# Optimization experiments

Hardware: AMD Instinct MI355X
Metric: run time of the kernel (lower is better)

Reference implementation:

```python
import jax, jax.numpy as jnp
import numpy as np


def _forward(agent_qs, ally_states, enemy_states, W_al, b_al, W_en, b_en, Wq, bq, Wk, bk,
             w1_W1, w1_b1, w1_W2, w1_b2, wf_W1, wf_b1, wf_W2, wf_b2, hb_W, hb_b,
             v_W1, v_b1, v_W2, v_b2):
    A, B, S, _ = ally_states.shape
    E = A + enemy_states.shape[0]
    D = W_al.shape[1]
    Da = Wq.shape[1]
    # entity encoders: [A,B,S,D], [En,B,S,D]
    ally_embed = ally_states @ W_al + b_al
    enemy_embed = enemy_states @ W_en + b_en
    entity = jnp.concatenate([ally_embed, enemy_embed], axis=0)      # [E,B,S,D]
    ent_bs = jnp.transpose(entity, (1, 2, 0, 3))                     # [B,S,E,D]
    q = ent_bs @ Wq + bq                                             # [B,S,E,Da]
    k = ent_bs @ Wk + bk                                             # [B,S,E,Da]
    scale = jnp.asarray(Da, q.dtype) ** 0.5
    energy = jnp.einsum('bsid,bsjd->bsij', q / scale, k)             # [B,S,E,E]
    # torch softmax(dim=1) on [BS,E,E] == softmax over the query axis i
    attn = jax.nn.softmax(energy, axis=2)
    # bmm(value[BS,D,E], attn).mean(-1) == value @ mean_j attn[:, :, e, j]
    attn_mean = jnp.mean(attn, axis=3)                               # [B,S,E]
    attn_out = jnp.einsum('bsed,bse->bsd', ent_bs, attn_mean)        # [B,S,D]
    ally_bs = jnp.transpose(ally_embed, (1, 2, 0, 3))                # [B,S,A,D]
    emi = jnp.concatenate(
        [jnp.broadcast_to(attn_out[:, :, None, :], (B, S, A, D)), ally_bs], axis=-1)  # [B,S,A,2D]
    # hypernets (2-layer)
    w1 = jnp.abs(jax.nn.relu(emi @ w1_W1 + w1_b1) @ w1_W2 + w1_b2)   # [B,S,A,M]
    b1 = attn_out @ hb_W + hb_b                                      # [B,S,M]
    hidden = jax.nn.elu(jnp.einsum('bsa,bsam->bsm', agent_qs, w1) + b1)
    wf = jnp.abs(jax.nn.relu(attn_out @ wf_W1 + wf_b1) @ wf_W2 + wf_b2)  # [B,S,M]
    v = jax.nn.relu(attn_out @ v_W1 + v_b1) @ v_W2 + v_b2            # [B,S,1]
    q_tot = jnp.einsum('bsm,bsm->bs', hidden, wf)[..., None] + v     # [B,S,1]
    return q_tot


def setup_inputs() -> dict:
    key = jax.random.key(0)
    B, S, A, En = 128, 128, 8, 8
    NFal, NFen, D, Da, M, H = 32, 16, 64, 128, 32, 64
    ks = jax.random.split(key, 32)
    p = lambda i, shape: jax.random.normal(ks[i], shape, dtype=jnp.float32) * 0.05
    return dict(
        agent_qs=jax.random.normal(ks[0], (B, S, A), dtype=jnp.float32),
        ally_states=jax.random.normal(ks[1], (A, B, S, NFal), dtype=jnp.float32),
        enemy_states=jax.random.normal(ks[2], (En, B, S, NFen), dtype=jnp.float32),
        W_al=p(3, (NFal, D)), b_al=p(4, (D,)), W_en=p(5, (NFen, D)), b_en=p(6, (D,)),
        Wq=p(7, (D, Da)), bq=p(8, (Da,)), Wk=p(9, (D, Da)), bk=p(10, (Da,)),
        w1_W1=p(11, (2 * D, H)), w1_b1=p(12, (H,)), w1_W2=p(13, (H, M)), w1_b2=p(14, (M,)),
        wf_W1=p(15, (D, H)), wf_b1=p(16, (H,)), wf_W2=p(17, (H, M)), wf_b2=p(18, (M,)),
        hb_W=p(19, (D, M)), hb_b=p(20, (M,)),
        v_W1=p(21, (D, M)), v_b1=p(22, (M,)), v_W2=p(23, (M, 1)), v_b2=p(24, (1,)),
    )


def reference(agent_qs, ally_states, enemy_states, W_al, b_al, W_en, b_en, Wq, bq, Wk, bk,
              w1_W1, w1_b1, w1_W2, w1_b2, wf_W1, wf_b1, wf_W2, wf_b2, hb_W, hb_b,
              v_W1, v_b1, v_W2, v_b2):
    return _forward(agent_qs, ally_states, enemy_states, W_al, b_al, W_en, b_en, Wq, bq, Wk, bk,
                    w1_W1, w1_b1, w1_W2, w1_b2, wf_W1, wf_b1, wf_W2, wf_b2, hb_W, hb_b,
                    v_W1, v_b1, v_W2, v_b2)
```

## Files before the change

### kernel.cpp

```cpp
#include <hip/hip_runtime.h>
#include <hip/hip_bf16.h>


#define B_   128
#define S_   128
#define BS_  (B_ * S_)
#define WPB  2
#define INV_S 0.08838834764831845f

typedef short bs8 __attribute__((ext_vector_type(8)));
typedef float f4  __attribute__((ext_vector_type(4)));

#define MFMA(a, b, c) __builtin_amdgcn_mfma_f32_16x16x32_bf16((a), (b), (c), 0, 0, 0)
#define LOADB(t) (*(const bs8*)&fb[(size_t)(t) * 512 + lane * 8])

__device__ __forceinline__ short f2bf(float f) {
    union { float f; unsigned u; } v; v.f = f;
    unsigned r = v.u + 0x7fffu + ((v.u >> 16) & 1u);
    return (short)(r >> 16);
}

__global__ __launch_bounds__(64)
void qmix_pre1(const float* __restrict__ Wq, const float* __restrict__ Wk,
               const float* __restrict__ bk,
               float* __restrict__ Ms, float* __restrict__ vq)
{
    const int blk = blockIdx.x, t = threadIdx.x;
    float p;
    if (blk < 4096) {
        const int k = blk >> 6, n = blk & 63;
        p = Wq[k * 128 + t] * Wk[n * 128 + t]
          + Wq[k * 128 + 64 + t] * Wk[n * 128 + 64 + t];
        #pragma unroll
        for (int off = 32; off >= 1; off >>= 1) p += __shfl_down(p, off, 64);
        if (t == 0) Ms[k * 64 + n] = p * INV_S;
    } else {
        const int d = blk - 4096;
        p = Wq[d * 128 + t] * bk[t] + Wq[d * 128 + 64 + t] * bk[64 + t];
        #pragma unroll
        for (int off = 32; off >= 1; off >>= 1) p += __shfl_down(p, off, 64);
        if (t == 0) vq[d] = p * INV_S;
    }
}

__global__ __launch_bounds__(64)
void qmix_pack(const float* __restrict__ Ms,
               const float* __restrict__ W_al, const float* __restrict__ W_en,
               const float* __restrict__ w1_W1, const float* __restrict__ w1_W2,
               const float* __restrict__ vq,
               const float* __restrict__ wf_W1, const float* __restrict__ hb_W,
               const float* __restrict__ v_W1,  const float* __restrict__ wf_W2,
               short* __restrict__ fb)
{
    const int blk = blockIdx.x, lane = threadIdx.x;
    const int quad = lane >> 4, l16 = lane & 15;
    bs8 v;
    if (blk < 8) {
        const int ks = blk >> 2, n = (blk & 3) * 16 + l16;
        #pragma unroll
        for (int j = 0; j < 8; ++j)
            v[j] = f2bf(Ms[(ks * 32 + quad * 8 + j) * 64 + n]);
    } else if (blk < 16) {
        const bool en = (blk >= 12);
        const float* W = en ? W_en : W_al;
        const int Krows = en ? 16 : 32;
        const int n = ((blk - (en ? 12 : 8)) & 3) * 16 + l16;
        #pragma unroll
        for (int j = 0; j < 8; ++j) {
            const int k = quad * 8 + j;
            v[j] = (k < Krows) ? f2bf(W[k * 64 + n]) : (short)0;
        }
    } else if (blk < 32) {
        const int t = blk - 16, ks = t >> 2, n = (t & 3) * 16 + l16;
        #pragma unroll
        for (int j = 0; j < 8; ++j)
            v[j] = f2bf(w1_W1[(ks * 32 + quad * 8 + j) * 64 + n]);
    } else if (blk < 36) {
        const int t = blk - 32, ks = t >> 1, n = (t & 1) * 16 + l16;
        #pragma unroll
        for (int j = 0; j < 8; ++j)
            v[j] = f2bf(w1_W2[(ks * 32 + quad * 8 + j) * 32 + n]);
    } else if (blk < 38) {
        const int ks = blk - 36;
        #pragma unroll
        for (int j = 0; j < 8; ++j)
            v[j] = (l16 == 0) ? f2bf(vq[ks * 32 + quad * 8 + j]) : (short)0;
    } else if (blk < 54) {
        const int t = blk - 38, ks = t >> 3, n = (t & 7) * 16 + l16;
        #pragma unroll
        for (int j = 0; j < 8; ++j) {
            const int k = ks * 32 + quad * 8 + j;
            float w;
            if (n < 64)       w = wf_W1[k * 64 + n];
            else if (n < 96)  w = hb_W[k * 32 + (n - 64)];
            else              w = v_W1[k * 32 + (n - 96)];
            v[j] = f2bf(w);
        }
    } else {
        const int t = blk - 54, ks = t >> 1, n = (t & 1) * 16 + l16;
        #pragma unroll
        for (int j = 0; j < 8; ++j)
            v[j] = f2bf(wf_W2[(ks * 32 + quad * 8 + j) * 32 + n]);
    }
    *(bs8*)&fb[(size_t)blk * 512 + lane * 8] = v;
}

struct __align__(16) WaveLds {
    short entb[16][72];
    short scr[16][72];
    short aoutb[64];
    short hb16[64];
    float qs[8];
};

__global__ __launch_bounds__(64 * WPB, 4)
void qmix_main(const float* __restrict__ agent_qs,
               const float* __restrict__ ally, const float* __restrict__ enemy,
               const float* __restrict__ b_al, const float* __restrict__ b_en,
               const float* __restrict__ w1_b1, const float* __restrict__ w1_b2,
               const float* __restrict__ wf_b1, const float* __restrict__ wf_b2,
               const float* __restrict__ hb_b,  const float* __restrict__ v_b1,
               const float* __restrict__ v_W2,  const float* __restrict__ v_b2,
               const short* __restrict__ fb,
               float* __restrict__ out)
{
    const int w    = threadIdx.x >> 6;
    const int lane = threadIdx.x & 63;
    const int site = blockIdx.x * WPB + w;
    const int quad = lane >> 4, l16 = lane & 15;

    __shared__ WaveLds lds[WPB];
    WaveLds& L = lds[w];

    if (lane < 8) L.qs[lane] = agent_qs[(size_t)site * 8 + lane];

    bs8 a_al = {0,0,0,0,0,0,0,0}, a_en = {0,0,0,0,0,0,0,0};
    if (l16 < 8) {
        const float* pa = ally + ((size_t)l16 * BS_ + site) * 32 + quad * 8;
        const float4 f0 = *(const float4*)pa, f1 = *(const float4*)(pa + 4);
        a_al[0]=f2bf(f0.x); a_al[1]=f2bf(f0.y); a_al[2]=f2bf(f0.z); a_al[3]=f2bf(f0.w);
        a_al[4]=f2bf(f1.x); a_al[5]=f2bf(f1.y); a_al[6]=f2bf(f1.z); a_al[7]=f2bf(f1.w);
    } else if (quad < 2) {
        const float* pe = enemy + ((size_t)(l16 - 8) * BS_ + site) * 16 + quad * 8;
        const float4 f0 = *(const float4*)pe, f1 = *(const float4*)(pe + 4);
        a_en[0]=f2bf(f0.x); a_en[1]=f2bf(f0.y); a_en[2]=f2bf(f0.z); a_en[3]=f2bf(f0.w);
        a_en[4]=f2bf(f1.x); a_en[5]=f2bf(f1.y); a_en[6]=f2bf(f1.z); a_en[7]=f2bf(f1.w);
    }

    f4 encf[4];
    #pragma unroll
    for (int n0t = 0; n0t < 4; ++n0t) {
        f4 acc = {0.f, 0.f, 0.f, 0.f};
        acc = MFMA(a_al, LOADB(8 + n0t), acc);
        acc = MFMA(a_en, LOADB(12 + n0t), acc);
        const int d = n0t * 16 + l16;
        const float bal = b_al[d], ben = b_en[d];
        #pragma unroll
        for (int r = 0; r < 4; ++r) {
            const int row = quad * 4 + r;
            const float v = acc[r] + (row < 8 ? bal : ben);
            encf[n0t][r] = v;
            L.entb[row][d] = f2bf(v);
        }
    }
    __syncthreads();

    const bs8 ae0 = *(const bs8*)&L.entb[l16][quad * 8];
    const bs8 ae1 = *(const bs8*)&L.entb[l16][32 + quad * 8];
    f4 pqacc = {0.f, 0.f, 0.f, 0.f};
    pqacc = MFMA(ae0, LOADB(36), pqacc);
    pqacc = MFMA(ae1, LOADB(37), pqacc);
    #pragma unroll
    for (int n0t = 0; n0t < 4; ++n0t) {
        f4 acc = {0.f, 0.f, 0.f, 0.f};
        acc = MFMA(ae0, LOADB(0 + n0t), acc);
        acc = MFMA(ae1, LOADB(4 + n0t), acc);
        const int d = n0t * 16 + l16;
        #pragma unroll
        for (int r = 0; r < 4; ++r) L.scr[quad * 4 + r][d] = f2bf(acc[r]);
    }
    __syncthreads();

    f4 eacc = {0.f, 0.f, 0.f, 0.f};
    {
        const bs8 at0 = *(const bs8*)&L.scr[l16][quad * 8];
        const bs8 at1 = *(const bs8*)&L.scr[l16][32 + quad * 8];
        eacc = MFMA(at0, ae0, eacc);
        eacc = MFMA(at1, ae1, eacc);
        const int src = lane & 48;
        #pragma unroll
        for (int r = 0; r < 4; ++r) eacc[r] += __shfl(pqacc[r], src, 64);
    }

    float amean_r[4];
    {
        float cmax = fmaxf(fmaxf(eacc[0], eacc[1]), fmaxf(eacc[2], eacc[3]));
        cmax = fmaxf(cmax, __shfl_xor(cmax, 16, 64));
        cmax = fmaxf(cmax, __shfl_xor(cmax, 32, 64));
        float er[4], csum = 0.f;
        #pragma unroll
        for (int r = 0; r < 4; ++r) { er[r] = __expf(eacc[r] - cmax); csum += er[r]; }
        csum += __shfl_xor(csum, 16, 64);
        csum += __shfl_xor(csum, 32, 64);
        const float inv = 1.f / csum;
        #pragma unroll
        for (int r = 0; r < 4; ++r) {
            float p = er[r] * inv;
            p += __shfl_xor(p, 1, 64);
            p += __shfl_xor(p, 2, 64);
            p += __shfl_xor(p, 4, 64);
            p += __shfl_xor(p, 8, 64);
            amean_r[r] = p * (1.f / 16.f);
        }
    }

    #pragma unroll
    for (int n0t = 0; n0t < 4; ++n0t) {
        float ap = amean_r[0] * encf[n0t][0] + amean_r[1] * encf[n0t][1]
                 + amean_r[2] * encf[n0t][2] + amean_r[3] * encf[n0t][3];
        ap += __shfl_xor(ap, 16, 64);
        ap += __shfl_xor(ap, 32, 64);
        if (quad == 0) L.aoutb[n0t * 16 + l16] = f2bf(ap);
    }
    __syncthreads();

    const bs8 a0 = *(const bs8*)&L.aoutb[quad * 8];
    const bs8 a1 = *(const bs8*)&L.aoutb[32 + quad * 8];

    float x[8];
    #pragma unroll
    for (int n0t = 0; n0t < 8; ++n0t) {
        f4 acc = {0.f, 0.f, 0.f, 0.f};
        acc = MFMA(a0, LOADB(38 + n0t), acc);
        acc = MFMA(a1, LOADB(46 + n0t), acc);
        x[n0t] = acc[0];
    }
    {
        const float xh = (quad == 0) ? x[0] : (quad == 1) ? x[1]
                       : (quad == 2) ? x[2] : x[3];
        L.hb16[lane] = f2bf(fmaxf(xh + wf_b1[lane], 0.f));
    }
    const float b1m = ((lane < 16) ? x[4] : x[5]) + ((lane < 32) ? hb_b[lane] : 0.f);
    float vsum;
    {
        float hv = fmaxf(x[6] + v_b1[l16], 0.f)      * v_W2[l16]
                 + fmaxf(x[7] + v_b1[16 + l16], 0.f) * v_W2[16 + l16];
        hv += __shfl_xor(hv, 1, 64);
        hv += __shfl_xor(hv, 2, 64);
        hv += __shfl_xor(hv, 4, 64);
        hv += __shfl_xor(hv, 8, 64);
        vsum = hv;
    }
    __syncthreads();

    float wfm;
    {
        const bs8 h0 = *(const bs8*)&L.hb16[quad * 8];
        const bs8 h1 = *(const bs8*)&L.hb16[32 + quad * 8];
        f4 acc0 = {0.f, 0.f, 0.f, 0.f};
        acc0 = MFMA(h0, LOADB(54), acc0);
        acc0 = MFMA(h1, LOADB(56), acc0);
        f4 acc1 = {0.f, 0.f, 0.f, 0.f};
        acc1 = MFMA(h0, LOADB(55), acc1);
        acc1 = MFMA(h1, LOADB(57), acc1);
        const float w0 = fabsf(acc0[0] + wf_b2[l16]);
        const float w1 = fabsf(acc1[0] + wf_b2[16 + l16]);
        wfm = (lane < 16) ? w0 : w1;
    }

    #pragma unroll
    for (int n0t = 0; n0t < 4; ++n0t) {
        f4 acc = {0.f, 0.f, 0.f, 0.f};
        acc = MFMA(a0,  LOADB(16 + 0 + n0t), acc);
        acc = MFMA(a1,  LOADB(16 + 4 + n0t), acc);
        acc = MFMA(ae0, LOADB(16 + 8 + n0t), acc);
        acc = MFMA(ae1, LOADB(16 + 12 + n0t), acc);
        const int d = n0t * 16 + l16;
        const float b1v = w1_b1[d];
        #pragma unroll
        for (int r = 0; r < 4; ++r) {
            const int row = quad * 4 + r;
            if (row < 8)
                L.scr[row][d] = f2bf(fmaxf(acc[r] + b1v, 0.f));
        }
    }
    __syncthreads();

    float p0 = 0.f, p1 = 0.f;
    {
        const bs8 ah0 = *(const bs8*)&L.scr[l16][quad * 8];
        const bs8 ah1 = *(const bs8*)&L.scr[l16][32 + quad * 8];
        #pragma unroll
        for (int n0t = 0; n0t < 2; ++n0t) {
            f4 acc = {0.f, 0.f, 0.f, 0.f};
            acc = MFMA(ah0, LOADB(32 + 0 + n0t), acc);
            acc = MFMA(ah1, LOADB(32 + 2 + n0t), acc);
            const int col = n0t * 16 + l16;
            const float b2v = w1_b2[col];
            float p = 0.f;
            if (quad < 2) {
                #pragma unroll
                for (int r = 0; r < 4; ++r)
                    p += L.qs[quad * 4 + r] * fabsf(acc[r] + b2v);
            }
            if (n0t == 0) p0 = p; else p1 = p;
        }
        p0 += __shfl_xor(p0, 16, 64);
        p1 += __shfl_xor(p1, 16, 64);
    }

    float contrib = 0.f;
    if (lane < 32) {
        float hp = (lane < 16 ? p0 : p1) + b1m;
        hp = (hp > 0.f) ? hp : (__expf(hp) - 1.f);
        contrib = hp * wfm;
    }
    #pragma unroll
    for (int off = 16; off >= 1; off >>= 1)
        contrib += __shfl_down(contrib, off, 64);
    if (lane == 0) out[site] = contrib + vsum + v_b2[0];
}

extern "C" void kernel_launch(void* const* d_in, const int* in_sizes, int n_in,
                              void* d_out, int out_size, void* d_ws, size_t ws_size,
                              hipStream_t stream) {
    const float* p[25];
    for (int i = 0; i < 25; ++i) p[i] = (const float*)d_in[i];
    short* fb = (short*)d_ws;
    float* vq = (float*)((char*)d_ws + 58 * 512 * 2);
    float* Ms = vq + 64;

    qmix_pre1<<<4096 + 64, 64, 0, stream>>>(p[7], p[9], p[10], Ms, vq);
    qmix_pack<<<58, 64, 0, stream>>>(Ms, p[3], p[5], p[11], p[13], vq,
                                     p[15], p[19], p[21], p[17], fb);
    qmix_main<<<BS_ / WPB, 64 * WPB, 0, stream>>>(
        p[0], p[1], p[2], p[4], p[6], p[12], p[14],
        p[16], p[18], p[20], p[22], p[23], p[24],
        fb, (float*)d_out);
}
```

Measured before the change: 163.2 us.

## Process two sites per wave and pack half-empty MFMA tiles across both sites

Each wave now handles two sites instead of one. The hypernet stages that previously wasted rows of the 16-row MFMA tiles (8 ally rows, a single attention-output row) now place both sites' data into one tile. This roughly halves the MFMA and weight-fragment loads per site in those stages, and the grid shrinks to a quarter of the site count. In exchange, per-wave register pressure rises (two sets of encodings and entity fragments) and the entity and attention stages stay serialized per site.

```diff
diff --git a/kernel.cpp b/kernel.cpp
--- a/kernel.cpp
+++ b/kernel.cpp
@@ -5,7 +5,6 @@
 #define B_   128
 #define S_   128
 #define BS_  (B_ * S_)
-#define WPB  2
 #define INV_S 0.08838834764831845f
 
 typedef short bs8 __attribute__((ext_vector_type(8)));
@@ -106,14 +105,13 @@
 }
 
 struct __align__(16) WaveLds {
-    short entb[16][72];
-    short scr[16][72];
-    short aoutb[64];
-    short hb16[64];
-    float qs[8];
+    short ent[2][16][72];
+    short aoutb[2][64];
+    short hb16[2][64];
+    float qs[2][8];
 };
 
-__global__ __launch_bounds__(64 * WPB, 4)
+__global__ __launch_bounds__(128, 4)
 void qmix_main(const float* __restrict__ agent_qs,
                const float* __restrict__ ally, const float* __restrict__ enemy,
                const float* __restrict__ b_al, const float* __restrict__ b_en,
@@ -126,74 +124,94 @@
 {
     const int w    = threadIdx.x >> 6;
     const int lane = threadIdx.x & 63;
-    const int site = blockIdx.x * WPB + w;
     const int quad = lane >> 4, l16 = lane & 15;
-
-    __shared__ WaveLds lds[WPB];
+    const int half = lane >> 5;
+    const int qh   = quad & 1;
+    const int siteA = blockIdx.x * 4 + w * 2;
+
+    __shared__ WaveLds lds[2];
     WaveLds& L = lds[w];
 
-    if (lane < 8) L.qs[lane] = agent_qs[(size_t)site * 8 + lane];
-
-    bs8 a_al = {0,0,0,0,0,0,0,0}, a_en = {0,0,0,0,0,0,0,0};
-    if (l16 < 8) {
-        const float* pa = ally + ((size_t)l16 * BS_ + site) * 32 + quad * 8;
-        const float4 f0 = *(const float4*)pa, f1 = *(const float4*)(pa + 4);
-        a_al[0]=f2bf(f0.x); a_al[1]=f2bf(f0.y); a_al[2]=f2bf(f0.z); a_al[3]=f2bf(f0.w);
-        a_al[4]=f2bf(f1.x); a_al[5]=f2bf(f1.y); a_al[6]=f2bf(f1.z); a_al[7]=f2bf(f1.w);
-    } else if (quad < 2) {
-        const float* pe = enemy + ((size_t)(l16 - 8) * BS_ + site) * 16 + quad * 8;
-        const float4 f0 = *(const float4*)pe, f1 = *(const float4*)(pe + 4);
-        a_en[0]=f2bf(f0.x); a_en[1]=f2bf(f0.y); a_en[2]=f2bf(f0.z); a_en[3]=f2bf(f0.w);
-        a_en[4]=f2bf(f1.x); a_en[5]=f2bf(f1.y); a_en[6]=f2bf(f1.z); a_en[7]=f2bf(f1.w);
-    }
-
-    f4 encf[4];
-    #pragma unroll
-    for (int n0t = 0; n0t < 4; ++n0t) {
-        f4 acc = {0.f, 0.f, 0.f, 0.f};
-        acc = MFMA(a_al, LOADB(8 + n0t), acc);
-        acc = MFMA(a_en, LOADB(12 + n0t), acc);
-        const int d = n0t * 16 + l16;
-        const float bal = b_al[d], ben = b_en[d];
-        #pragma unroll
-        for (int r = 0; r < 4; ++r) {
-            const int row = quad * 4 + r;
-            const float v = acc[r] + (row < 8 ? bal : ben);
-            encf[n0t][r] = v;
-            L.entb[row][d] = f2bf(v);
-        }
-    }
-    __syncthreads();
-
-    const bs8 ae0 = *(const bs8*)&L.entb[l16][quad * 8];
-    const bs8 ae1 = *(const bs8*)&L.entb[l16][32 + quad * 8];
-    f4 pqacc = {0.f, 0.f, 0.f, 0.f};
-    pqacc = MFMA(ae0, LOADB(36), pqacc);
-    pqacc = MFMA(ae1, LOADB(37), pqacc);
-    #pragma unroll
-    for (int n0t = 0; n0t < 4; ++n0t) {
-        f4 acc = {0.f, 0.f, 0.f, 0.f};
-        acc = MFMA(ae0, LOADB(0 + n0t), acc);
-        acc = MFMA(ae1, LOADB(4 + n0t), acc);
-        const int d = n0t * 16 + l16;
-        #pragma unroll
-        for (int r = 0; r < 4; ++r) L.scr[quad * 4 + r][d] = f2bf(acc[r]);
-    }
-    __syncthreads();
-
-    f4 eacc = {0.f, 0.f, 0.f, 0.f};
-    {
-        const bs8 at0 = *(const bs8*)&L.scr[l16][quad * 8];
-        const bs8 at1 = *(const bs8*)&L.scr[l16][32 + quad * 8];
-        eacc = MFMA(at0, ae0, eacc);
-        eacc = MFMA(at1, ae1, eacc);
-        const int src = lane & 48;
-        #pragma unroll
-        for (int r = 0; r < 4; ++r) eacc[r] += __shfl(pqacc[r], src, 64);
-    }
-
-    float amean_r[4];
-    {
+    if (lane < 16)
+        L.qs[lane >> 3][lane & 7] =
+            agent_qs[(size_t)(siteA + (lane >> 3)) * 8 + (lane & 7)];
+
+    f4 encf[2][4];
+    #pragma unroll
+    for (int s = 0; s < 2; ++s) {
+        const int site = siteA + s;
+        bs8 a_al = {0,0,0,0,0,0,0,0}, a_en = {0,0,0,0,0,0,0,0};
+        if (l16 < 8) {
+            const float* pa = ally + ((size_t)l16 * BS_ + site) * 32 + quad * 8;
+            const float4 f0 = *(const float4*)pa, f1 = *(const float4*)(pa + 4);
+            a_al[0]=f2bf(f0.x); a_al[1]=f2bf(f0.y); a_al[2]=f2bf(f0.z); a_al[3]=f2bf(f0.w);
+            a_al[4]=f2bf(f1.x); a_al[5]=f2bf(f1.y); a_al[6]=f2bf(f1.z); a_al[7]=f2bf(f1.w);
+        } else if (quad < 2) {
+            const float* pe = enemy + ((size_t)(l16 - 8) * BS_ + site) * 16 + quad * 8;
+            const float4 f0 = *(const float4*)pe, f1 = *(const float4*)(pe + 4);
+            a_en[0]=f2bf(f0.x); a_en[1]=f2bf(f0.y); a_en[2]=f2bf(f0.z); a_en[3]=f2bf(f0.w);
+            a_en[4]=f2bf(f1.x); a_en[5]=f2bf(f1.y); a_en[6]=f2bf(f1.z); a_en[7]=f2bf(f1.w);
+        }
+        #pragma unroll
+        for (int n0t = 0; n0t < 4; ++n0t) {
+            f4 acc = {0.f, 0.f, 0.f, 0.f};
+            acc = MFMA(a_al, LOADB(8 + n0t), acc);
+            acc = MFMA(a_en, LOADB(12 + n0t), acc);
+            const int d = n0t * 16 + l16;
+            const float bal = b_al[d], ben = b_en[d];
+            #pragma unroll
+            for (int r = 0; r < 4; ++r) {
+                const int row = quad * 4 + r;
+                const float v = acc[r] + (row < 8 ? bal : ben);
+                encf[s][n0t][r] = v;
+                L.ent[s][row][d] = f2bf(v);
+            }
+        }
+    }
+    __syncthreads();
+
+    bs8 ae0s[2], ae1s[2];
+    #pragma unroll
+    for (int s = 0; s < 2; ++s) {
+        ae0s[s] = *(const bs8*)&L.ent[s][l16][quad * 8];
+        ae1s[s] = *(const bs8*)&L.ent[s][l16][32 + quad * 8];
+    }
+    const short (*entP)[72] = (l16 < 8) ? L.ent[0] : L.ent[1];
+    const bs8 ag0 = *(const bs8*)&entP[l16 & 7][quad * 8];
+    const bs8 ag1 = *(const bs8*)&entP[l16 & 7][32 + quad * 8];
+    __syncthreads();
+
+    f4 pqs[2];
+    #pragma unroll
+    for (int s = 0; s < 2; ++s) {
+        f4 pq = {0.f, 0.f, 0.f, 0.f};
+        pq = MFMA(ae0s[s], LOADB(36), pq);
+        pq = MFMA(ae1s[s], LOADB(37), pq);
+        pqs[s] = pq;
+        #pragma unroll
+        for (int n0t = 0; n0t < 4; ++n0t) {
+            f4 acc = {0.f, 0.f, 0.f, 0.f};
+            acc = MFMA(ae0s[s], LOADB(0 + n0t), acc);
+            acc = MFMA(ae1s[s], LOADB(4 + n0t), acc);
+            const int d = n0t * 16 + l16;
+            #pragma unroll
+            for (int r = 0; r < 4; ++r) L.ent[s][quad * 4 + r][d] = f2bf(acc[r]);
+        }
+    }
+    __syncthreads();
+
+    #pragma unroll
+    for (int s = 0; s < 2; ++s) {
+        f4 eacc = {0.f, 0.f, 0.f, 0.f};
+        {
+            const bs8 at0 = *(const bs8*)&L.ent[s][l16][quad * 8];
+            const bs8 at1 = *(const bs8*)&L.ent[s][l16][32 + quad * 8];
+            eacc = MFMA(at0, ae0s[s], eacc);
+            eacc = MFMA(at1, ae1s[s], eacc);
+            const int src = lane & 48;
+            #pragma unroll
+            for (int r = 0; r < 4; ++r) eacc[r] += __shfl(pqs[s][r], src, 64);
+        }
         float cmax = fmaxf(fmaxf(eacc[0], eacc[1]), fmaxf(eacc[2], eacc[3]));
         cmax = fmaxf(cmax, __shfl_xor(cmax, 16, 64));
         cmax = fmaxf(cmax, __shfl_xor(cmax, 32, 64));
@@ -203,6 +221,7 @@
         csum += __shfl_xor(csum, 16, 64);
         csum += __shfl_xor(csum, 32, 64);
         const float inv = 1.f / csum;
+        float amean[4];
         #pragma unroll
         for (int r = 0; r < 4; ++r) {
             float p = er[r] * inv;
@@ -210,115 +229,112 @@
             p += __shfl_xor(p, 2, 64);
             p += __shfl_xor(p, 4, 64);
             p += __shfl_xor(p, 8, 64);
-            amean_r[r] = p * (1.f / 16.f);
-        }
-    }
-
-    #pragma unroll
-    for (int n0t = 0; n0t < 4; ++n0t) {
-        float ap = amean_r[0] * encf[n0t][0] + amean_r[1] * encf[n0t][1]
-                 + amean_r[2] * encf[n0t][2] + amean_r[3] * encf[n0t][3];
-        ap += __shfl_xor(ap, 16, 64);
-        ap += __shfl_xor(ap, 32, 64);
-        if (quad == 0) L.aoutb[n0t * 16 + l16] = f2bf(ap);
-    }
-    __syncthreads();
-
-    const bs8 a0 = *(const bs8*)&L.aoutb[quad * 8];
-    const bs8 a1 = *(const bs8*)&L.aoutb[32 + quad * 8];
-
-    float x[8];
+            amean[r] = p * (1.f / 16.f);
+        }
+        #pragma unroll
+        for (int n0t = 0; n0t < 4; ++n0t) {
+            float ap = amean[0] * encf[s][n0t][0] + amean[1] * encf[s][n0t][1]
+                     + amean[2] * encf[s][n0t][2] + amean[3] * encf[s][n0t][3];
+            ap += __shfl_xor(ap, 16, 64);
+            ap += __shfl_xor(ap, 32, 64);
+            if (quad == 0) L.aoutb[s][n0t * 16 + l16] = f2bf(ap);
+        }
+    }
+    __syncthreads();
+
+    const short* aoP = L.aoutb[l16 >> 3];
+    const bs8 aab0 = *(const bs8*)&aoP[quad * 8];
+    const bs8 aab1 = *(const bs8*)&aoP[32 + quad * 8];
+
+    float xm[8];
     #pragma unroll
     for (int n0t = 0; n0t < 8; ++n0t) {
         f4 acc = {0.f, 0.f, 0.f, 0.f};
-        acc = MFMA(a0, LOADB(38 + n0t), acc);
-        acc = MFMA(a1, LOADB(46 + n0t), acc);
-        x[n0t] = acc[0];
-    }
-    {
-        const float xh = (quad == 0) ? x[0] : (quad == 1) ? x[1]
-                       : (quad == 2) ? x[2] : x[3];
-        L.hb16[lane] = f2bf(fmaxf(xh + wf_b1[lane], 0.f));
-    }
-    const float b1m = ((lane < 16) ? x[4] : x[5]) + ((lane < 32) ? hb_b[lane] : 0.f);
+        acc = MFMA(aab0, LOADB(38 + n0t), acc);
+        acc = MFMA(aab1, LOADB(46 + n0t), acc);
+        xm[n0t] = acc[0];
+    }
+    #pragma unroll
+    for (int n0t = 0; n0t < 4; ++n0t) {
+        const int t = n0t * 16 + l16;
+        L.hb16[half][t] = f2bf(fmaxf(xm[n0t] + wf_b1[t], 0.f));
+    }
+    const int m32 = lane & 31;
+    const float b1m = xm[4 + qh] + hb_b[m32];
     float vsum;
     {
-        float hv = fmaxf(x[6] + v_b1[l16], 0.f)      * v_W2[l16]
-                 + fmaxf(x[7] + v_b1[16 + l16], 0.f) * v_W2[16 + l16];
+        float hv = fmaxf(xm[6 + qh] + v_b1[m32], 0.f) * v_W2[m32];
         hv += __shfl_xor(hv, 1, 64);
         hv += __shfl_xor(hv, 2, 64);
         hv += __shfl_xor(hv, 4, 64);
         hv += __shfl_xor(hv, 8, 64);
+        hv += __shfl_xor(hv, 16, 64);
         vsum = hv;
     }
     __syncthreads();
 
     float wfm;
     {
-        const bs8 h0 = *(const bs8*)&L.hb16[quad * 8];
-        const bs8 h1 = *(const bs8*)&L.hb16[32 + quad * 8];
+        const short* hfP = L.hb16[l16 >> 3];
+        const bs8 hf0 = *(const bs8*)&hfP[quad * 8];
+        const bs8 hf1 = *(const bs8*)&hfP[32 + quad * 8];
         f4 acc0 = {0.f, 0.f, 0.f, 0.f};
-        acc0 = MFMA(h0, LOADB(54), acc0);
-        acc0 = MFMA(h1, LOADB(56), acc0);
+        acc0 = MFMA(hf0, LOADB(54), acc0);
+        acc0 = MFMA(hf1, LOADB(56), acc0);
         f4 acc1 = {0.f, 0.f, 0.f, 0.f};
-        acc1 = MFMA(h0, LOADB(55), acc1);
-        acc1 = MFMA(h1, LOADB(57), acc1);
-        const float w0 = fabsf(acc0[0] + wf_b2[l16]);
-        const float w1 = fabsf(acc1[0] + wf_b2[16 + l16]);
-        wfm = (lane < 16) ? w0 : w1;
+        acc1 = MFMA(hf0, LOADB(55), acc1);
+        acc1 = MFMA(hf1, LOADB(57), acc1);
+        wfm = fabsf((qh ? acc1[0] : acc0[0]) + wf_b2[m32]);
     }
 
     #pragma unroll
     for (int n0t = 0; n0t < 4; ++n0t) {
         f4 acc = {0.f, 0.f, 0.f, 0.f};
-        acc = MFMA(a0,  LOADB(16 + 0 + n0t), acc);
-        acc = MFMA(a1,  LOADB(16 + 4 + n0t), acc);
-        acc = MFMA(ae0, LOADB(16 + 8 + n0t), acc);
-        acc = MFMA(ae1, LOADB(16 + 12 + n0t), acc);
+        acc = MFMA(aab0, LOADB(16 + 0 + n0t), acc);
+        acc = MFMA(aab1, LOADB(16 + 4 + n0t), acc);
+        acc = MFMA(ag0,  LOADB(16 + 8 + n0t), acc);
+        acc = MFMA(ag1,  LOADB(16 + 12 + n0t), acc);
         const int d = n0t * 16 + l16;
         const float b1v = w1_b1[d];
         #pragma unroll
-        for (int r = 0; r < 4; ++r) {
-            const int row = quad * 4 + r;
-            if (row < 8)
-                L.scr[row][d] = f2bf(fmaxf(acc[r] + b1v, 0.f));
-        }
-    }
-    __syncthreads();
-
-    float p0 = 0.f, p1 = 0.f;
+        for (int r = 0; r < 4; ++r)
+            L.ent[0][quad * 4 + r][d] = f2bf(fmaxf(acc[r] + b1v, 0.f));
+    }
+    __syncthreads();
+
+    float pm;
     {
-        const bs8 ah0 = *(const bs8*)&L.scr[l16][quad * 8];
-        const bs8 ah1 = *(const bs8*)&L.scr[l16][32 + quad * 8];
+        const bs8 ha0 = *(const bs8*)&L.ent[0][l16][quad * 8];
+        const bs8 ha1 = *(const bs8*)&L.ent[0][l16][32 + quad * 8];
+        const float* qsv = L.qs[half];
+        float p0 = 0.f, p1 = 0.f;
         #pragma unroll
         for (int n0t = 0; n0t < 2; ++n0t) {
             f4 acc = {0.f, 0.f, 0.f, 0.f};
-            acc = MFMA(ah0, LOADB(32 + 0 + n0t), acc);
-            acc = MFMA(ah1, LOADB(32 + 2 + n0t), acc);
-            const int col = n0t * 16 + l16;
-            const float b2v = w1_b2[col];
+            acc = MFMA(ha0, LOADB(32 + 0 + n0t), acc);
+            acc = MFMA(ha1, LOADB(32 + 2 + n0t), acc);
+            const float b2v = w1_b2[n0t * 16 + l16];
             float p = 0.f;
-            if (quad < 2) {
-                #pragma unroll
-                for (int r = 0; r < 4; ++r)
-                    p += L.qs[quad * 4 + r] * fabsf(acc[r] + b2v);
-            }
+            #pragma unroll
+            for (int r = 0; r < 4; ++r)
+                p += qsv[qh * 4 + r] * fabsf(acc[r] + b2v);
             if (n0t == 0) p0 = p; else p1 = p;
         }
         p0 += __shfl_xor(p0, 16, 64);
         p1 += __shfl_xor(p1, 16, 64);
-    }
-
-    float contrib = 0.f;
-    if (lane < 32) {
-        float hp = (lane < 16 ? p0 : p1) + b1m;
-        hp = (hp > 0.f) ? hp : (__expf(hp) - 1.f);
-        contrib = hp * wfm;
-    }
-    #pragma unroll
-    for (int off = 16; off >= 1; off >>= 1)
-        contrib += __shfl_down(contrib, off, 64);
-    if (lane == 0) out[site] = contrib + vsum + v_b2[0];
+        pm = qh ? p1 : p0;
+    }
+
+    float hp = pm + b1m;
+    hp = (hp > 0.f) ? hp : (__expf(hp) - 1.f);
+    float contrib = hp * wfm;
+    contrib += __shfl_xor(contrib, 1, 64);
+    contrib += __shfl_xor(contrib, 2, 64);
+    contrib += __shfl_xor(contrib, 4, 64);
+    contrib += __shfl_xor(contrib, 8, 64);
+    contrib += __shfl_xor(contrib, 16, 64);
+    if ((lane & 31) == 0)
+        out[siteA + half] = contrib + vsum + v_b2[0];
 }
 
 extern "C" void kernel_launch(void* const* d_in, const int* in_sizes, int n_in,
@@ -333,7 +349,7 @@
     qmix_pre1<<<4096 + 64, 64, 0, stream>>>(p[7], p[9], p[10], Ms, vq);
     qmix_pack<<<58, 64, 0, stream>>>(Ms, p[3], p[5], p[11], p[13], vq,
                                      p[15], p[19], p[21], p[17], fb);
-    qmix_main<<<BS_ / WPB, 64 * WPB, 0, stream>>>(
+    qmix_main<<<BS_ / 4, 128, 0, stream>>>(
         p[0], p[1], p[2], p[4], p[6], p[12], p[14],
         p[16], p[18], p[20], p[22], p[23], p[24],
         fb, (float*)d_out);
```

New measurement: 155.0 us. -5.0%, faster.
